# Kernel tuning notes

Hardware: AMD Instinct MI355X
Metric: run time of the kernel (lower is better)

The kernel has to match this reference:

```python
import jax, jax.numpy as jnp
import numpy as np

G, R = 2, 2          # heterogeneous graphs, meta-paths per node type
ND = NT = 3072       # drug / target node counts
NHEADS = 8
E = 100000           # DTI pairs
NEG = -1e9


def setup_inputs() -> dict:
    key = jax.random.key(0)
    ks = jax.random.split(key, 32)

    def rn(k, shape):
        return (jax.random.normal(k, shape) / np.sqrt(shape[0])).astype(jnp.float32)

    inp = {
        'x_drug': jax.random.normal(ks[0], (ND, 1024), dtype=jnp.float32),
        'x_target': jax.random.normal(ks[1], (NT, 1280), dtype=jnp.float32),
        'bias_drug': jnp.where(jax.random.uniform(ks[2], (G, R, ND, ND)) < 0.02, 0.0, NEG).astype(jnp.float32),
        'bias_target': jnp.where(jax.random.uniform(ks[3], (G, R, NT, NT)) < 0.02, 0.0, NEG).astype(jnp.float32),
        'edge_index': jax.random.randint(ks[4], (2, E), 0, ND, dtype=jnp.int64),
        'dnn_w1': rn(ks[5], (1024, 512)), 'dnn_b1': jnp.zeros((512,), jnp.float32),
        'dnn_w2': rn(ks[6], (512, 256)), 'dnn_b2': jnp.zeros((256,), jnp.float32),
        'dnn_w3': rn(ks[7], (256, 128)), 'dnn_b3': jnp.zeros((128,), jnp.float32),
        'tnn_w1': rn(ks[8], (1280, 512)), 'tnn_b1': jnp.zeros((512,), jnp.float32),
        'tnn_w2': rn(ks[9], (512, 256)), 'tnn_b2': jnp.zeros((256,), jnp.float32),
        'tnn_w3': rn(ks[10], (256, 128)), 'tnn_b3': jnp.zeros((128,), jnp.float32),
        'gat_w': rn(ks[11], (128, 16)),
        'gat_a1': rn(ks[12], (16, 1)),
        'gat_a2': rn(ks[13], (16, 1)),
        'att_w': rn(ks[14], (128, 128)), 'att_b': jnp.zeros((128,), jnp.float32),
        'att_u': rn(ks[15], (128,)),
        'a_omega': rn(ks[16], (128, 1)),
        'dec_w1': rn(ks[17], (256, 64)), 'dec_b1': jnp.zeros((64,), jnp.float32),
        'dec_w2': rn(ks[18], (64, 1)), 'dec_b2': jnp.zeros((1,), jnp.float32),
    }
    return inp


def reference(x_drug, x_target, bias_drug, bias_target, edge_index,
              dnn_w1, dnn_b1, dnn_w2, dnn_b2, dnn_w3, dnn_b3,
              tnn_w1, tnn_b1, tnn_w2, tnn_b2, tnn_w3, tnn_b3,
              gat_w, gat_a1, gat_a2, att_w, att_b, att_u, a_omega,
              dec_w1, dec_b1, dec_w2, dec_b2):

    def mlp3(x, w1, b1, w2, b2, w3, b3):  # feature NN (eval mode)
        h = jax.nn.relu(x @ w1 + b1)
        h = jax.nn.relu(h @ w2 + b2)
        return jax.nn.relu(h @ w3 + b3)

    def branch(feats, bias):
        # feats [N,128], bias [G,R,N,N]. Shared GAT layer + dropout off -> all heads identical.
        wh = feats @ gat_w                                                  # [N,16]
        e = jax.nn.leaky_relu(wh @ gat_a1 + (wh @ gat_a2).T, 0.2)           # [N,N]
        att = jax.nn.softmax(e[None, None] + bias, axis=-1)                 # [G,R,N,N]
        head = jax.nn.elu(jnp.einsum('grnm,md->grnd', att, wh))             # [G,R,N,16]
        multi = jnp.swapaxes(jnp.tile(head, (1, 1, 1, NHEADS)), 1, 2)       # [G,N,R,128]
        # semantic (meta-path) attention per graph
        v = jnp.tanh(multi @ att_w + att_b)                                 # [G,N,R,128]
        alphas = jax.nn.softmax(v @ att_u, axis=-1)                         # [G,N,R]
        per_graph = jnp.einsum('gnrh,gnr->gnh', multi, alphas)              # [G,N,128]
        # combine across heterogeneous graphs with a_omega + softmax(dim=0)
        w = jax.nn.softmax(jnp.mean(per_graph @ a_omega, axis=(1, 2)), axis=0)  # [G]
        return jnp.einsum('g,gnh->nh', w, per_graph)                        # [N,128]

    final_drug = branch(mlp3(x_drug, dnn_w1, dnn_b1, dnn_w2, dnn_b2, dnn_w3, dnn_b3), bias_drug)
    final_target = branch(mlp3(x_target, tnn_w1, tnn_b1, tnn_w2, tnn_b2, tnn_w3, tnn_b3), bias_target)

    # DTI decoder on edge pairs
    h = jnp.concatenate([final_drug[edge_index[0]], final_target[edge_index[1]]], axis=-1)  # [E,256]
    h = jax.nn.relu(h @ dec_w1 + dec_b1)
    return jax.nn.sigmoid(h @ dec_w2 + dec_b2).reshape(-1)
```

## Files before the change

### kernel.cpp

```cpp
#include <hip/hip_runtime.h>
#include <math.h>

#define ND 3072
#define EDG 100000
#define MAXE 128
#define BSL (64*8 + 16)

typedef __attribute__((ext_vector_type(8))) short short8;
typedef __attribute__((ext_vector_type(4))) float f32x4;

enum : size_t {
  OFF_FEATD = 0,
  OFF_FEATT = OFF_FEATD + 393216,
  OFF_WHD   = OFF_FEATT + 393216,
  OFF_WHT   = OFF_WHD + 49152,
  OFF_S1D   = OFF_WHT + 49152,
  OFF_S2D   = OFF_S1D + 3072,
  OFF_S1T   = OFF_S2D + 3072,
  OFF_S2T   = OFF_S1T + 3072,
  OFF_HEADD = OFF_S2T + 3072,
  OFF_HEADT = OFF_HEADD + 196608,
  OFF_PGD   = OFF_HEADT + 196608,
  OFF_PGT   = OFF_PGD + 98304,
  OFF_F16D  = OFF_PGT + 98304,
  OFF_F16T  = OFF_F16D + 49152,
  OFF_AWS   = OFF_F16T + 49152,
  OFF_W1D   = OFF_AWS + 2048,
  OFF_W1T   = OFF_W1D + 1024,
  OFF_AOM   = OFF_W1T + 1024,
  OFF_DOTSD = OFF_AOM + 16,
  OFF_DOTST = OFF_DOTSD + 6144,
  OFF_GSUM  = OFF_DOTST + 6144,
  OFF_S2MD  = OFF_GSUM + 4,
  OFF_S2MT  = OFF_S2MD + 1,
  OFF_W1DH  = ((OFF_S2MT + 4) & ~(size_t)3),
  OFF_W1DL  = OFF_W1DH + 262144,
  OFF_W1TH  = OFF_W1DL + 262144,
  OFF_W1TL  = OFF_W1TH + 327680,
  OFF_W2DH  = OFF_W1TL + 327680,
  OFF_W2DL  = OFF_W2DH + 65536,
  OFF_W2TH  = OFF_W2DL + 65536,
  OFF_W2TL  = OFF_W2TH + 65536,
  OFF_W3DH  = OFF_W2TL + 65536,
  OFF_W3DL  = OFF_W3DH + 16384,
  OFF_W3TH  = OFF_W3DL + 16384,
  OFF_W3TL  = OFF_W3TH + 16384,
  OFF_XDH   = OFF_W3TL + 16384,
  OFF_XDL   = OFF_XDH + 1572864,
  OFF_XTH   = OFF_XDL + 1572864,
  OFF_XTL   = OFF_XTH + 1966080,
  OFF_H1DH  = OFF_XTL + 1966080,
  OFF_H1DL  = OFF_H1DH + 786432,
  OFF_H1TH  = OFF_H1DL + 786432,
  OFF_H1TL  = OFF_H1TH + 786432,
  OFF_H2DH  = OFF_H1TL + 786432,
  OFF_H2DL  = OFF_H2DH + 393216,
  OFF_H2TH  = OFF_H2DL + 393216,
  OFF_H2TL  = OFF_H2TH + 393216,
  WS_GRAND  = OFF_H2TL + 393216
};

__device__ __forceinline__ ushort f2bf(float f) {
  union { float f; unsigned u; } v; v.f = f;
  unsigned r = (v.u + 0x7fffu + ((v.u >> 16) & 1u)) >> 16;
  return (ushort)r;
}
__device__ __forceinline__ float bf2f(ushort h) {
  union { float f; unsigned u; } v; v.u = ((unsigned)h) << 16;
  return v.f;
}

__global__ __launch_bounds__(256) void prep_all(
    const float* __restrict__ w1d, const float* __restrict__ w1t,
    const float* __restrict__ w2d, const float* __restrict__ w2t,
    const float* __restrict__ w3d, const float* __restrict__ w3t,
    const float* __restrict__ xd,  const float* __restrict__ xt,
    const float* __restrict__ att_w, const float* __restrict__ dec_w1,
    const float* __restrict__ a_omega, float* __restrict__ ws)
{
  const int b = blockIdx.x, t = threadIdx.x;
  if (b < 736) {
    const float* W; ushort* hi; ushort* lo; int nsh, base;
    if (b < 256)      { W=w1d; hi=(ushort*)(ws+OFF_W1DH); lo=(ushort*)(ws+OFF_W1DL); nsh=9; base=0; }
    else if (b < 576) { W=w1t; hi=(ushort*)(ws+OFF_W1TH); lo=(ushort*)(ws+OFF_W1TL); nsh=9; base=256; }
    else if (b < 640) { W=w2d; hi=(ushort*)(ws+OFF_W2DH); lo=(ushort*)(ws+OFF_W2DL); nsh=8; base=576; }
    else if (b < 704) { W=w2t; hi=(ushort*)(ws+OFF_W2TH); lo=(ushort*)(ws+OFF_W2TL); nsh=8; base=640; }
    else if (b < 720) { W=w3d; hi=(ushort*)(ws+OFF_W3DH); lo=(ushort*)(ws+OFF_W3DL); nsh=7; base=704; }
    else              { W=w3t; hi=(ushort*)(ws+OFF_W3TH); lo=(ushort*)(ws+OFF_W3TL); nsh=7; base=720; }
    const int u = (b - base)*256 + t;
    const int k8 = u >> nsh;
    const int n  = u & ((1 << nsh) - 1);
    __align__(16) ushort h8[8], l8[8];
    #pragma unroll
    for (int j2 = 0; j2 < 8; ++j2) {
      float x = W[(size_t)(k8*8 + j2) * (1 << nsh) + n];
      ushort h = f2bf(x);
      h8[j2] = h; l8[j2] = f2bf(x - bf2f(h));
    }
    *(uint4*)&hi[(size_t)u*8] = *(const uint4*)h8;
    *(uint4*)&lo[(size_t)u*8] = *(const uint4*)l8;
  } else if (b < 7648) {
    const float* X; ushort* hi; ushort* lo; int base;
    if (b < 3808) { X=xd; hi=(ushort*)(ws+OFF_XDH); lo=(ushort*)(ws+OFF_XDL); base=736; }
    else          { X=xt; hi=(ushort*)(ws+OFF_XTH); lo=(ushort*)(ws+OFF_XTL); base=3808; }
    const size_t u = ((size_t)(b-base)*256 + t)*4;
    float4 v = *(const float4*)&X[u];
    ushort4 h, l;
    h.x=f2bf(v.x); l.x=f2bf(v.x-bf2f(h.x));
    h.y=f2bf(v.y); l.y=f2bf(v.y-bf2f(h.y));
    h.z=f2bf(v.z); l.z=f2bf(v.z-bf2f(h.z));
    h.w=f2bf(v.w); l.w=f2bf(v.w-bf2f(h.w));
    *(ushort4*)&hi[u] = h; *(ushort4*)&lo[u] = l;
  } else if (b == 7648) {
    float* aws = ws + OFF_AWS; float* aom = ws + OFF_AOM;
    for (int i = t; i < 2048; i += 256) {
      int d = i >> 7, o = i & 127;
      float sum = 0.f;
      #pragma unroll
      for (int tt = 0; tt < 8; ++tt) sum += att_w[(tt*16 + d)*128 + o];
      aws[i] = sum;
    }
    if (t < 16) {
      float sum = 0.f;
      #pragma unroll
      for (int tt = 0; tt < 8; ++tt) sum += a_omega[tt*16 + t];
      aom[t] = sum;
    }
  } else {
    float* W1d = ws + OFF_W1D; float* W1t = ws + OFF_W1T;
    for (int i = t; i < 1024; i += 256) {
      int d = i >> 6, o = i & 63;
      float sd = 0.f, st = 0.f;
      #pragma unroll
      for (int tt = 0; tt < 8; ++tt) {
        sd += dec_w1[(tt*16 + d)*64 + o];
        st += dec_w1[(128 + tt*16 + d)*64 + o];
      }
      W1d[i] = sd; W1t[i] = st;
    }
  }
}

template<int BM, int EPI>
__global__ __launch_bounds__(256) void mfma_gemm2(
    const ushort* __restrict__ A0h, const ushort* __restrict__ A0l,
    const ushort* __restrict__ B0h, const ushort* __restrict__ B0l,
    const float* __restrict__ b0, float* __restrict__ C0f,
    ushort* __restrict__ C0h, ushort* __restrict__ C0l,
    const ushort* __restrict__ A1h, const ushort* __restrict__ A1l,
    const ushort* __restrict__ B1h, const ushort* __restrict__ B1l,
    const float* __restrict__ b1, float* __restrict__ C1f,
    ushort* __restrict__ C1h, ushort* __restrict__ C1l,
    int N, int K0, int K1)
{
  constexpr int ASLT = BM*8 + 16;
  constexpr int NP   = 3072 / BM;
  constexpr int AI   = BM / 32;
  __shared__ __align__(16) ushort Ah[8*ASLT], Al[8*ASLT];
  __shared__ __align__(16) ushort Bh[8*BSL], Bl[8*BSL];
  const int t = threadIdx.x;
  const int lane = t & 63, w = t >> 6;
  const int wr = w >> 1, wc = w & 1;
  const int l15 = lane & 15, l4 = lane >> 4;

  const int id = blockIdx.y * gridDim.x + blockIdx.x;
  const int xcd = id & 7;
  const int j = id >> 3;
  const int bx = j % gridDim.x;
  const int by = (j / gridDim.x) * 8 + xcd;
  const int half = by >= NP;
  const int row0 = (half ? by - NP : by) * BM;
  const int col0 = bx << 6;
  const ushort* Ahi = half ? A1h : A0h; const ushort* Alo = half ? A1l : A0l;
  const ushort* Bhi = half ? B1h : B0h; const ushort* Blo = half ? B1l : B0l;
  const float* bias = half ? b1 : b0;
  float* Cf = half ? C1f : C0f;
  ushort* Chi = half ? C1h : C0h; ushort* Clo = half ? C1l : C0l;
  const int K = half ? K1 : K0;

  f32x4 acc[AI][2] = {};

  const int arow = t >> 3;
  const int akc  = t & 7;
  const int bkc  = t >> 6;
  const int bcol = t & 63;

  uint4 sa0, sa1, sa2, sa3, sl0, sl1, sl2, sl3, sb0, sb1, sc0, sc1;

#define GLOAD(k0_) { \
    size_t g0 = (size_t)(row0 + arow) * K + (k0_) + (akc << 3); \
    sa0 = *(const uint4*)(Ahi + g0);                     sl0 = *(const uint4*)(Alo + g0); \
    sa1 = *(const uint4*)(Ahi + g0 + 32*(size_t)K);      sl1 = *(const uint4*)(Alo + g0 + 32*(size_t)K); \
    if (AI > 2) { \
      sa2 = *(const uint4*)(Ahi + g0 + 64*(size_t)K);    sl2 = *(const uint4*)(Alo + g0 + 64*(size_t)K); \
      sa3 = *(const uint4*)(Ahi + g0 + 96*(size_t)K);    sl3 = *(const uint4*)(Alo + g0 + 96*(size_t)K); \
    } \
    size_t gb0 = ((size_t)(((k0_) >> 3) + bkc    ) * N + col0 + bcol) << 3; \
    size_t gb1 = ((size_t)(((k0_) >> 3) + bkc + 4) * N + col0 + bcol) << 3; \
    sb0 = *(const uint4*)(Bhi + gb0); sc0 = *(const uint4*)(Blo + gb0); \
    sb1 = *(const uint4*)(Bhi + gb1); sc1 = *(const uint4*)(Blo + gb1); \
  }

#define LDSW() { \
    int ao = akc * ASLT + arow * 8; \
    *(uint4*)&Ah[ao      ] = sa0;  *(uint4*)&Al[ao      ] = sl0; \
    *(uint4*)&Ah[ao + 256] = sa1;  *(uint4*)&Al[ao + 256] = sl1; \
    if (AI > 2) { \
      *(uint4*)&Ah[ao + 512] = sa2;  *(uint4*)&Al[ao + 512] = sl2; \
      *(uint4*)&Ah[ao + 768] = sa3;  *(uint4*)&Al[ao + 768] = sl3; \
    } \
    int bo = bkc * BSL + bcol * 8; \
    *(uint4*)&Bh[bo        ] = sb0; *(uint4*)&Bl[bo        ] = sc0; \
    *(uint4*)&Bh[bo + 4*BSL] = sb1; *(uint4*)&Bl[bo + 4*BSL] = sc1; \
  }

  GLOAD(0);
  for (int k0 = 0; k0 < K; k0 += 64) {
    __syncthreads();
    LDSW();
    __syncthreads();
    if (k0 + 64 < K) GLOAD(k0 + 64);
    #pragma unroll
    for (int ks = 0; ks < 2; ++ks) {
      const int kch = (ks << 2) + l4;
      const int bbase = kch * BSL + ((wc << 5) + l15) * 8;
      short8 fb0 = *(const short8*)&Bh[bbase];
      short8 fb1 = *(const short8*)&Bh[bbase + 128];
      short8 gl0 = *(const short8*)&Bl[bbase];
      short8 gl1 = *(const short8*)&Bl[bbase + 128];
      #pragma unroll
      for (int m = 0; m < AI; ++m) {
        const int abase = kch * ASLT + (wr*(BM/2) + (m << 4) + l15) * 8;
        short8 fa = *(const short8*)&Ah[abase];
        short8 fl = *(const short8*)&Al[abase];
        acc[m][0] = __builtin_amdgcn_mfma_f32_16x16x32_bf16(fa, fb0, acc[m][0], 0, 0, 0);
        acc[m][0] = __builtin_amdgcn_mfma_f32_16x16x32_bf16(fa, gl0, acc[m][0], 0, 0, 0);
        acc[m][0] = __builtin_amdgcn_mfma_f32_16x16x32_bf16(fl, fb0, acc[m][0], 0, 0, 0);
        acc[m][1] = __builtin_amdgcn_mfma_f32_16x16x32_bf16(fa, fb1, acc[m][1], 0, 0, 0);
        acc[m][1] = __builtin_amdgcn_mfma_f32_16x16x32_bf16(fa, gl1, acc[m][1], 0, 0, 0);
        acc[m][1] = __builtin_amdgcn_mfma_f32_16x16x32_bf16(fl, fb1, acc[m][1], 0, 0, 0);
      }
    }
  }
#undef GLOAD
#undef LDSW

  #pragma unroll
  for (int n = 0; n < 2; ++n) {
    int col = col0 + (wc << 5) + (n << 4) + l15;
    float bb = bias[col];
    #pragma unroll
    for (int m = 0; m < AI; ++m) {
      int rowb = row0 + wr*(BM/2) + (m << 4) + (l4 << 2);
      #pragma unroll
      for (int r = 0; r < 4; ++r) {
        float v = fmaxf(acc[m][n][r] + bb, 0.f);
        size_t d = (size_t)(rowb + r) * N + col;
        if (EPI == 0) {
          Cf[d] = v;
        } else {
          ushort h = f2bf(v);
          Chi[d] = h;
          Clo[d] = f2bf(v - bf2f(h));
        }
      }
    }
  }
}

__global__ __launch_bounds__(256) void wh_kernel(const float* __restrict__ featD,
    const float* __restrict__ featT,
    const float* __restrict__ gw, const float* __restrict__ ga1, const float* __restrict__ ga2,
    float* __restrict__ ws)
{
  __shared__ float W[128*16];
  __shared__ float A1[16], A2[16];
  const int t = threadIdx.x;
  const int half = blockIdx.x >= 192;
  const float* feat = half ? featT : featD;
  float* wh = ws + (half ? OFF_WHT : OFF_WHD);
  float* s1 = ws + (half ? OFF_S1T : OFF_S1D);
  float* s2 = ws + (half ? OFF_S2T : OFF_S2D);
  const int bid = half ? blockIdx.x - 192 : blockIdx.x;
  for (int i = t; i < 2048; i += 256) W[i] = gw[i];
  if (t < 16) { A1[t] = ga1[t]; A2[t] = ga2[t]; }
  __syncthreads();
  const int n = (bid << 4) + (t >> 4);
  const int d = t & 15;
  const float* f = feat + (size_t)n * 128;
  float acc = 0.f;
  #pragma unroll 8
  for (int k = 0; k < 128; ++k) acc += f[k] * W[k*16 + d];
  wh[(size_t)n*16 + d] = acc;
  float v1 = acc * A1[d], v2 = acc * A2[d];
  #pragma unroll
  for (int off = 8; off; off >>= 1) { v1 += __shfl_xor(v1, off); v2 += __shfl_xor(v2, off); }
  if (d == 0) { s1[n] = v1; s2[n] = v2; }
}

__global__ __launch_bounds__(256) void max_kernel(float* __restrict__ ws)
{
  const int t = threadIdx.x;
  const float* s2 = ws + (blockIdx.x ? OFF_S2T : OFF_S2D);
  float* out = ws + (blockIdx.x ? OFF_S2MT : OFF_S2MD);
  float m = -INFINITY;
  for (int i = t; i < ND; i += 256) m = fmaxf(m, s2[i]);
  #pragma unroll
  for (int off = 32; off; off >>= 1) m = fmaxf(m, __shfl_xor(m, off));
  __shared__ float red[4];
  if ((t & 63) == 0) red[t >> 6] = m;
  __syncthreads();
  if (t == 0) out[0] = fmaxf(fmaxf(red[0], red[1]), fmaxf(red[2], red[3]));
}

__global__ __launch_bounds__(256) void scan_kernel(const float* __restrict__ bias_d,
    const float* __restrict__ bias_t, float* __restrict__ ws)
{
  const int half = blockIdx.x >= 3072;
  const float* bias = half ? bias_t : bias_d;
  unsigned short* idx = (unsigned short*)(ws + (half ? OFF_H1TH : OFF_H1DH));
  int* cnts = (int*)(ws + (half ? OFF_H2TH : OFF_H2DH));
  const int bid = half ? blockIdx.x - 3072 : blockIdx.x;
  const int lane = threadIdx.x & 63;
  const int row = (bid << 2) + (threadIdx.x >> 6);
  const f32x4* brow = (const f32x4*)(bias + (size_t)row * ND);
  unsigned short* ei = idx + (size_t)row * MAXE;
  const unsigned long long ltmask = (1ull << lane) - 1ull;
  int cnt = 0;
  #pragma unroll 3
  for (int i = 0; i < ND/256; ++i) {
    const int j4 = lane + (i << 6);
    f32x4 b = __builtin_nontemporal_load(&brow[j4]);
    #pragma unroll
    for (int c = 0; c < 4; ++c) {
      float bv = b[c];
      bool e = bv > -1e8f;
      unsigned long long mask = __ballot(e);
      if (e) {
        int pos = cnt + __popcll(mask & ltmask);
        if (pos < MAXE) ei[pos] = (unsigned short)((j4 << 2) + c);
      }
      cnt += __popcll(mask);
    }
  }
  if (lane == 0) cnts[row] = cnt < MAXE ? cnt : MAXE;
}

__global__ __launch_bounds__(256) void acc_kernel(float* __restrict__ ws)
{
  const int half = blockIdx.x >= 3072;
  const unsigned short* idx = (const unsigned short*)(ws + (half ? OFF_H1TH : OFF_H1DH));
  const int* cnts = (const int*)(ws + (half ? OFF_H2TH : OFF_H2DH));
  const float* s1 = ws + (half ? OFF_S1T : OFF_S1D);
  const float* s2 = ws + (half ? OFF_S2T : OFF_S2D);
  const float* s2max = ws + (half ? OFF_S2MT : OFF_S2MD);
  const float* wh = ws + (half ? OFF_WHT : OFF_WHD);
  float* head = ws + (half ? OFF_HEADT : OFF_HEADD);
  const int bid = half ? blockIdx.x - 3072 : blockIdx.x;
  const int lane = threadIdx.x & 63;
  const int row = (bid << 2) + (threadIdx.x >> 6);
  const int n = row % ND;
  const int eg = lane >> 4, d = lane & 15;
  const float s1v = s1[n];
  float mn = s1v + s2max[0];
  mn = (mn >= 0.f) ? mn : 0.2f * mn;
  const unsigned short* ei = idx + (size_t)row * MAXE;
  const int cnt = cnts[row];
  float acc = 0.f, ss = 0.f;
  if (cnt > 0) {
    for (int slot = eg; slot < cnt; slot += 4) {
      int j = ei[slot];
      float x = s1v + s2[j];
      x = (x >= 0.f) ? x : 0.2f * x;
      float p = __expf(x - mn);
      ss += p;
      acc += p * wh[j*16 + d];
    }
  } else {
    for (int j = eg; j < ND; j += 4) {
      float x = s1v + s2[j];
      x = (x >= 0.f) ? x : 0.2f * x;
      float p = __expf(x - mn);
      ss += p;
      acc += p * wh[j*16 + d];
    }
  }
  acc += __shfl_xor(acc, 16); acc += __shfl_xor(acc, 32);
  ss  += __shfl_xor(ss, 16);  ss  += __shfl_xor(ss, 32);
  if (lane < 16) {
    float v = acc / ss;
    head[(size_t)row * 16 + lane] = (v > 0.f) ? v : expm1f(v);
  }
}

__global__ __launch_bounds__(256) void sem_kernel(const float* __restrict__ att_b,
    const float* __restrict__ att_u, float* __restrict__ ws)
{
  __shared__ float AWS[2048];
  __shared__ float AB[128], AU[128], AOM[16];
  __shared__ float hsh[2][2][16];
  __shared__ float wred[4][2];
  const int half = blockIdx.x >= 3072;
  const float* head = ws + (half ? OFF_HEADT : OFF_HEADD);
  float* pg = ws + (half ? OFF_PGT : OFF_PGD);
  float* dots = ws + (half ? OFF_DOTST : OFF_DOTSD);
  const float* aws = ws + OFF_AWS;
  const float* aom = ws + OFF_AOM;
  const int bid = half ? blockIdx.x - 3072 : blockIdx.x;
  const int t = threadIdx.x;
  for (int i = t; i < 2048; i += 256) AWS[i] = aws[i];
  if (t < 128) { AB[t] = att_b[t]; AU[t] = att_u[t]; }
  if (t < 16) AOM[t] = aom[t];
  const int grp = t >> 7, o = t & 127;
  const int gn = (bid << 1) + grp;
  const int g = gn / ND, n = gn % ND;
  if (o < 32) {
    int r = o >> 4, d = o & 15;
    hsh[grp][r][d] = head[((size_t)(g*2 + r) * ND + n) * 16 + d];
  }
  __syncthreads();
  #pragma unroll
  for (int r = 0; r < 2; ++r) {
    float a = AB[o];
    #pragma unroll
    for (int d = 0; d < 16; ++d) a += hsh[grp][r][d] * AWS[d*128 + o];
    float v = tanhf(a) * AU[o];
    #pragma unroll
    for (int off = 32; off; off >>= 1) v += __shfl_xor(v, off);
    if ((t & 63) == 0) wred[t >> 6][r] = v;
  }
  __syncthreads();
  float t0 = wred[grp*2][0] + wred[grp*2 + 1][0];
  float t1 = wred[grp*2][1] + wred[grp*2 + 1][1];
  float mx = fmaxf(t0, t1);
  float e0 = __expf(t0 - mx), e1 = __expf(t1 - mx);
  float inv = 1.f / (e0 + e1);
  float a0 = e0 * inv, a1 = e1 * inv;
  if (o < 16) {
    float pv = a0 * hsh[grp][0][o] + a1 * hsh[grp][1][o];
    pg[((size_t)g * ND + n) * 16 + o] = pv;
    float contrib = pv * AOM[o];
    #pragma unroll
    for (int off = 8; off; off >>= 1) contrib += __shfl_xor(contrib, off);
    if (o == 0) dots[(size_t)g * ND + n] = contrib;
  }
}

__global__ __launch_bounds__(256) void reduce_gsum(float* __restrict__ ws)
{
  const int b = blockIdx.x, t = threadIdx.x;
  const float* dots = ws + (b < 2 ? OFF_DOTSD : OFF_DOTST) + (size_t)(b & 1) * ND;
  float v = 0.f;
  for (int i = t; i < ND; i += 256) v += dots[i];
  __shared__ float red[4];
  #pragma unroll
  for (int off = 32; off; off >>= 1) v += __shfl_xor(v, off);
  if ((t & 63) == 0) red[t >> 6] = v;
  __syncthreads();
  if (t == 0) ws[OFF_GSUM + b] = red[0] + red[1] + red[2] + red[3];
}

__global__ __launch_bounds__(256) void finalize_kernel(float* __restrict__ ws)
{
  const int half = blockIdx.x >= 192;
  const float* pg = ws + (half ? OFF_PGT : OFF_PGD);
  const float* gsum = ws + OFF_GSUM + half*2;
  float* f16 = ws + (half ? OFF_F16T : OFF_F16D);
  const int bid = half ? blockIdx.x - 192 : blockIdx.x;
  float g0 = gsum[0] * (1.f/ND), g1 = gsum[1] * (1.f/ND);
  float mx = fmaxf(g0, g1);
  float e0 = __expf(g0 - mx), e1 = __expf(g1 - mx);
  float w0 = e0 / (e0 + e1), w1 = e1 / (e0 + e1);
  int i = bid * 256 + threadIdx.x;
  if (i < ND*16) f16[i] = w0 * pg[i] + w1 * pg[ND*16 + i];
}

__global__ __launch_bounds__(256) void dec_kernel(const int* __restrict__ ei,
    const float* __restrict__ ws, const float* __restrict__ b1,
    const float* __restrict__ w2, const float* __restrict__ b2,
    float* __restrict__ out)
{
  __shared__ float WdT[64][16], WtT[64][16];
  __shared__ float B1[64], W2s[64];
  const float* f16d = ws + OFF_F16D;
  const float* f16t = ws + OFF_F16T;
  const float* W1d = ws + OFF_W1D;
  const float* W1t = ws + OFF_W1T;
  const int t = threadIdx.x;
  for (int i = t; i < 1024; i += 256) {
    int d = i >> 6, o = i & 63;
    WdT[o][d] = W1d[i];
    WtT[o][d] = W1t[i];
  }
  if (t < 64) { B1[t] = b1[t]; W2s[t] = w2[t]; }
  __syncthreads();
  const int e = blockIdx.x * 256 + t;
  if (e >= EDG) return;
  const int i0 = ei[e], i1 = ei[EDG + e];
  const float4* pd = (const float4*)(f16d + (size_t)i0 * 16);
  const float4* pt = (const float4*)(f16t + (size_t)i1 * 16);
  float4 d0 = pd[0], d1 = pd[1], d2 = pd[2], d3 = pd[3];
  float4 e0 = pt[0], e1 = pt[1], e2 = pt[2], e3 = pt[3];
  float outv = b2[0];
  #pragma unroll 4
  for (int o = 0; o < 64; ++o) {
    const float4* wd = (const float4*)&WdT[o][0];
    const float4* wt = (const float4*)&WtT[o][0];
    float4 wd0 = wd[0], wd1 = wd[1], wd2 = wd[2], wd3 = wd[3];
    float4 wt0 = wt[0], wt1 = wt[1], wt2 = wt[2], wt3 = wt[3];
    float a = B1[o];
    a += d0.x*wd0.x + d0.y*wd0.y + d0.z*wd0.z + d0.w*wd0.w;
    a += d1.x*wd1.x + d1.y*wd1.y + d1.z*wd1.z + d1.w*wd1.w;
    a += d2.x*wd2.x + d2.y*wd2.y + d2.z*wd2.z + d2.w*wd2.w;
    a += d3.x*wd3.x + d3.y*wd3.y + d3.z*wd3.z + d3.w*wd3.w;
    a += e0.x*wt0.x + e0.y*wt0.y + e0.z*wt0.z + e0.w*wt0.w;
    a += e1.x*wt1.x + e1.y*wt1.y + e1.z*wt1.z + e1.w*wt1.w;
    a += e2.x*wt2.x + e2.y*wt2.y + e2.z*wt2.z + e2.w*wt2.w;
    a += e3.x*wt3.x + e3.y*wt3.y + e3.z*wt3.z + e3.w*wt3.w;
    a = fmaxf(a, 0.f);
    outv += a * W2s[o];
  }
  out[e] = 1.f / (1.f + __expf(-outv));
}

extern "C" void kernel_launch(void* const* d_in, const int* in_sizes, int n_in,
                              void* d_out, int out_size, void* d_ws, size_t ws_size,
                              hipStream_t stream)
{
  const float* x_drug   = (const float*)d_in[0];
  const float* x_target = (const float*)d_in[1];
  const float* bias_d   = (const float*)d_in[2];
  const float* bias_t   = (const float*)d_in[3];
  const int*   ei       = (const int*)d_in[4];
  const float* dnn_w1 = (const float*)d_in[5];  const float* dnn_b1 = (const float*)d_in[6];
  const float* dnn_w2 = (const float*)d_in[7];  const float* dnn_b2 = (const float*)d_in[8];
  const float* dnn_w3 = (const float*)d_in[9];  const float* dnn_b3 = (const float*)d_in[10];
  const float* tnn_w1 = (const float*)d_in[11]; const float* tnn_b1 = (const float*)d_in[12];
  const float* tnn_w2 = (const float*)d_in[13]; const float* tnn_b2 = (const float*)d_in[14];
  const float* tnn_w3 = (const float*)d_in[15]; const float* tnn_b3 = (const float*)d_in[16];
  const float* gat_w  = (const float*)d_in[17];
  const float* gat_a1 = (const float*)d_in[18];
  const float* gat_a2 = (const float*)d_in[19];
  const float* att_w  = (const float*)d_in[20];
  const float* att_b  = (const float*)d_in[21];
  const float* att_u  = (const float*)d_in[22];
  const float* a_omega= (const float*)d_in[23];
  const float* dec_w1 = (const float*)d_in[24]; const float* dec_b1 = (const float*)d_in[25];
  const float* dec_w2 = (const float*)d_in[26]; const float* dec_b2 = (const float*)d_in[27];
  float* out = (float*)d_out;
  float* ws = (float*)d_ws;

  ushort* w1dh = (ushort*)(ws + OFF_W1DH); ushort* w1dl = (ushort*)(ws + OFF_W1DL);
  ushort* w1th = (ushort*)(ws + OFF_W1TH); ushort* w1tl = (ushort*)(ws + OFF_W1TL);
  ushort* w2dh = (ushort*)(ws + OFF_W2DH); ushort* w2dl = (ushort*)(ws + OFF_W2DL);
  ushort* w2th = (ushort*)(ws + OFF_W2TH); ushort* w2tl = (ushort*)(ws + OFF_W2TL);
  ushort* w3dh = (ushort*)(ws + OFF_W3DH); ushort* w3dl = (ushort*)(ws + OFF_W3DL);
  ushort* w3th = (ushort*)(ws + OFF_W3TH); ushort* w3tl = (ushort*)(ws + OFF_W3TL);
  ushort* xdh  = (ushort*)(ws + OFF_XDH);  ushort* xdl  = (ushort*)(ws + OFF_XDL);
  ushort* xth  = (ushort*)(ws + OFF_XTH);  ushort* xtl  = (ushort*)(ws + OFF_XTL);
  ushort* h1dh = (ushort*)(ws + OFF_H1DH); ushort* h1dl = (ushort*)(ws + OFF_H1DL);
  ushort* h1th = (ushort*)(ws + OFF_H1TH); ushort* h1tl = (ushort*)(ws + OFF_H1TL);
  ushort* h2dh = (ushort*)(ws + OFF_H2DH); ushort* h2dl = (ushort*)(ws + OFF_H2DL);
  ushort* h2th = (ushort*)(ws + OFF_H2TH); ushort* h2tl = (ushort*)(ws + OFF_H2TL);
  float* featD = ws + OFF_FEATD;
  float* featT = ws + OFF_FEATT;

  prep_all<<<7650, 256, 0, stream>>>(dnn_w1, tnn_w1, dnn_w2, tnn_w2, dnn_w3, tnn_w3,
      x_drug, x_target, att_w, dec_w1, a_omega, ws);

  mfma_gemm2<128,1><<<dim3(8,48), 256, 0, stream>>>(
      xdh, xdl, w1dh, w1dl, dnn_b1, nullptr, h1dh, h1dl,
      xth, xtl, w1th, w1tl, tnn_b1, nullptr, h1th, h1tl, 512, 1024, 1280);
  mfma_gemm2<64,1><<<dim3(4,96), 256, 0, stream>>>(
      h1dh, h1dl, w2dh, w2dl, dnn_b2, nullptr, h2dh, h2dl,
      h1th, h1tl, w2th, w2tl, tnn_b2, nullptr, h2th, h2tl, 256, 512, 512);
  mfma_gemm2<64,0><<<dim3(2,96), 256, 0, stream>>>(
      h2dh, h2dl, w3dh, w3dl, dnn_b3, featD, nullptr, nullptr,
      h2th, h2tl, w3th, w3tl, tnn_b3, featT, nullptr, nullptr, 128, 256, 256);

  wh_kernel<<<384, 256, 0, stream>>>(featD, featT, gat_w, gat_a1, gat_a2, ws);
  max_kernel<<<2, 256, 0, stream>>>(ws);

  scan_kernel<<<6144, 256, 0, stream>>>(bias_d, bias_t, ws);
  acc_kernel<<<6144, 256, 0, stream>>>(ws);

  sem_kernel<<<6144, 256, 0, stream>>>(att_b, att_u, ws);
  reduce_gsum<<<4, 256, 0, stream>>>(ws);
  finalize_kernel<<<384, 256, 0, stream>>>(ws);

  dec_kernel<<<(EDG + 255) / 256, 256, 0, stream>>>(ei, ws, dec_b1, dec_w2, dec_b2, out);
}
```

Baseline: 212.5 us.

## Use direct global-to-LDS loads in GEMM and fold tiny reduction kernels away

The split-bf16 GEMM now stages A and B tiles with global_load_lds 16-byte direct copies into LDS, using an XOR-swizzled A layout instead of register staging. Because the old double-buffered register prefetch is gone, a barrier now ends each k-step. The s2 max is computed with an order-preserving uint atomicMax inside wh_kernel, which replaces max_kernel. The gsum reduction is recomputed redundantly in every finalize block, which replaces reduce_gsum. Together these drop two launches and register-staging overhead, at the cost of losing load/compute overlap in the GEMM loop.

Result: slower. 221.6 us (+4.3%).

```diff
diff --git a/kernel.cpp b/kernel.cpp
--- a/kernel.cpp
+++ b/kernel.cpp
@@ -4,7 +4,6 @@
 #define ND 3072
 #define EDG 100000
 #define MAXE 128
-#define BSL (64*8 + 16)
 
 typedef __attribute__((ext_vector_type(8))) short short8;
 typedef __attribute__((ext_vector_type(4))) float f32x4;
@@ -30,8 +29,7 @@
   OFF_AOM   = OFF_W1T + 1024,
   OFF_DOTSD = OFF_AOM + 16,
   OFF_DOTST = OFF_DOTSD + 6144,
-  OFF_GSUM  = OFF_DOTST + 6144,
-  OFF_S2MD  = OFF_GSUM + 4,
+  OFF_S2MD  = OFF_DOTST + 6144,
   OFF_S2MT  = OFF_S2MD + 1,
   OFF_W1DH  = ((OFF_S2MT + 4) & ~(size_t)3),
   OFF_W1DL  = OFF_W1DH + 262144,
@@ -70,6 +68,12 @@
   return v.f;
 }
 
+__device__ __forceinline__ void gld16(const ushort* g, ushort* s) {
+  __builtin_amdgcn_global_load_lds(
+      (const __attribute__((address_space(1))) unsigned int*)(const void*)g,
+      (__attribute__((address_space(3))) unsigned int*)(void*)s, 16, 0, 0);
+}
+
 __global__ __launch_bounds__(256) void prep_all(
     const float* __restrict__ w1d, const float* __restrict__ w1t,
     const float* __restrict__ w2d, const float* __restrict__ w2t,
@@ -126,6 +130,10 @@
       for (int tt = 0; tt < 8; ++tt) sum += a_omega[tt*16 + t];
       aom[t] = sum;
     }
+    if (t == 0) {
+      ((unsigned*)(ws + OFF_S2MD))[0] = 0u;
+      ((unsigned*)(ws + OFF_S2MT))[0] = 0u;
+    }
   } else {
     float* W1d = ws + OFF_W1D; float* W1t = ws + OFF_W1T;
     for (int i = t; i < 1024; i += 256) {
@@ -153,11 +161,12 @@
     ushort* __restrict__ C1h, ushort* __restrict__ C1l,
     int N, int K0, int K1)
 {
-  constexpr int ASLT = BM*8 + 16;
   constexpr int NP   = 3072 / BM;
   constexpr int AI   = BM / 32;
-  __shared__ __align__(16) ushort Ah[8*ASLT], Al[8*ASLT];
-  __shared__ __align__(16) ushort Bh[8*BSL], Bl[8*BSL];
+  constexpr int AGW  = BM / 32;
+  constexpr int BSLU = 512 + 16;
+  __shared__ __align__(16) ushort Ah[BM*64], Al[BM*64];
+  __shared__ __align__(16) ushort Bh[8*BSLU], Bl[8*BSLU];
   const int t = threadIdx.x;
   const int lane = t & 63, w = t >> 6;
   const int wr = w >> 1, wc = w & 1;
@@ -180,59 +189,40 @@
 
   f32x4 acc[AI][2] = {};
 
-  const int arow = t >> 3;
-  const int akc  = t & 7;
-  const int bkc  = t >> 6;
-  const int bcol = t & 63;
-
-  uint4 sa0, sa1, sa2, sa3, sl0, sl1, sl2, sl3, sb0, sb1, sc0, sc1;
-
-#define GLOAD(k0_) { \
-    size_t g0 = (size_t)(row0 + arow) * K + (k0_) + (akc << 3); \
-    sa0 = *(const uint4*)(Ahi + g0);                     sl0 = *(const uint4*)(Alo + g0); \
-    sa1 = *(const uint4*)(Ahi + g0 + 32*(size_t)K);      sl1 = *(const uint4*)(Alo + g0 + 32*(size_t)K); \
-    if (AI > 2) { \
-      sa2 = *(const uint4*)(Ahi + g0 + 64*(size_t)K);    sl2 = *(const uint4*)(Alo + g0 + 64*(size_t)K); \
-      sa3 = *(const uint4*)(Ahi + g0 + 96*(size_t)K);    sl3 = *(const uint4*)(Alo + g0 + 96*(size_t)K); \
-    } \
-    size_t gb0 = ((size_t)(((k0_) >> 3) + bkc    ) * N + col0 + bcol) << 3; \
-    size_t gb1 = ((size_t)(((k0_) >> 3) + bkc + 4) * N + col0 + bcol) << 3; \
-    sb0 = *(const uint4*)(Bhi + gb0); sc0 = *(const uint4*)(Blo + gb0); \
-    sb1 = *(const uint4*)(Bhi + gb1); sc1 = *(const uint4*)(Blo + gb1); \
-  }
-
-#define LDSW() { \
-    int ao = akc * ASLT + arow * 8; \
-    *(uint4*)&Ah[ao      ] = sa0;  *(uint4*)&Al[ao      ] = sl0; \
-    *(uint4*)&Ah[ao + 256] = sa1;  *(uint4*)&Al[ao + 256] = sl1; \
-    if (AI > 2) { \
-      *(uint4*)&Ah[ao + 512] = sa2;  *(uint4*)&Al[ao + 512] = sl2; \
-      *(uint4*)&Ah[ao + 768] = sa3;  *(uint4*)&Al[ao + 768] = sl3; \
-    } \
-    int bo = bkc * BSL + bcol * 8; \
-    *(uint4*)&Bh[bo        ] = sb0; *(uint4*)&Bl[bo        ] = sc0; \
-    *(uint4*)&Bh[bo + 4*BSL] = sb1; *(uint4*)&Bl[bo + 4*BSL] = sc1; \
-  }
-
-  GLOAD(0);
+  const int arg = lane >> 3;
+  const int slt = lane & 7;
+  const int kcd = slt ^ arg;
+
   for (int k0 = 0; k0 < K; k0 += 64) {
+    #pragma unroll
+    for (int i = 0; i < AGW; ++i) {
+      const int g = w + (i << 2);
+      const size_t ga = (size_t)(row0 + (g << 3) + arg) * K + k0 + (kcd << 3);
+      gld16(Ahi + ga, &Ah[g << 9]);
+      gld16(Alo + ga, &Al[g << 9]);
+    }
+    #pragma unroll
+    for (int i = 0; i < 2; ++i) {
+      const int kc = w + (i << 2);
+      const size_t gb = ((size_t)((k0 >> 3) + kc) * N + col0 + lane) << 3;
+      gld16(Bhi + gb, &Bh[kc * BSLU]);
+      gld16(Blo + gb, &Bl[kc * BSLU]);
+    }
     __syncthreads();
-    LDSW();
-    __syncthreads();
-    if (k0 + 64 < K) GLOAD(k0 + 64);
     #pragma unroll
     for (int ks = 0; ks < 2; ++ks) {
       const int kch = (ks << 2) + l4;
-      const int bbase = kch * BSL + ((wc << 5) + l15) * 8;
-      short8 fb0 = *(const short8*)&Bh[bbase];
-      short8 fb1 = *(const short8*)&Bh[bbase + 128];
-      short8 gl0 = *(const short8*)&Bl[bbase];
-      short8 gl1 = *(const short8*)&Bl[bbase + 128];
+      const int bb = kch * BSLU + ((wc << 5) + l15) * 8;
+      short8 fb0 = *(const short8*)&Bh[bb];
+      short8 fb1 = *(const short8*)&Bh[bb + 128];
+      short8 gl0 = *(const short8*)&Bl[bb];
+      short8 gl1 = *(const short8*)&Bl[bb + 128];
       #pragma unroll
       for (int m = 0; m < AI; ++m) {
-        const int abase = kch * ASLT + (wr*(BM/2) + (m << 4) + l15) * 8;
-        short8 fa = *(const short8*)&Ah[abase];
-        short8 fl = *(const short8*)&Al[abase];
+        const int R = wr*(BM/2) + (m << 4) + l15;
+        const int ab = (R << 6) + ((kch ^ (R & 7)) << 3);
+        short8 fa = *(const short8*)&Ah[ab];
+        short8 fl = *(const short8*)&Al[ab];
         acc[m][0] = __builtin_amdgcn_mfma_f32_16x16x32_bf16(fa, fb0, acc[m][0], 0, 0, 0);
         acc[m][0] = __builtin_amdgcn_mfma_f32_16x16x32_bf16(fa, gl0, acc[m][0], 0, 0, 0);
         acc[m][0] = __builtin_amdgcn_mfma_f32_16x16x32_bf16(fl, fb0, acc[m][0], 0, 0, 0);
@@ -241,9 +231,8 @@
         acc[m][1] = __builtin_amdgcn_mfma_f32_16x16x32_bf16(fl, fb1, acc[m][1], 0, 0, 0);
       }
     }
-  }
-#undef GLOAD
-#undef LDSW
+    __syncthreads();
+  }
 
   #pragma unroll
   for (int n = 0; n < 2; ++n) {
@@ -281,6 +270,7 @@
   float* wh = ws + (half ? OFF_WHT : OFF_WHD);
   float* s1 = ws + (half ? OFF_S1T : OFF_S1D);
   float* s2 = ws + (half ? OFF_S2T : OFF_S2D);
+  unsigned* s2m = (unsigned*)(ws + (half ? OFF_S2MT : OFF_S2MD));
   const int bid = half ? blockIdx.x - 192 : blockIdx.x;
   for (int i = t; i < 2048; i += 256) W[i] = gw[i];
   if (t < 16) { A1[t] = ga1[t]; A2[t] = ga2[t]; }
@@ -295,22 +285,12 @@
   float v1 = acc * A1[d], v2 = acc * A2[d];
   #pragma unroll
   for (int off = 8; off; off >>= 1) { v1 += __shfl_xor(v1, off); v2 += __shfl_xor(v2, off); }
-  if (d == 0) { s1[n] = v1; s2[n] = v2; }
-}
-
-__global__ __launch_bounds__(256) void max_kernel(float* __restrict__ ws)
-{
-  const int t = threadIdx.x;
-  const float* s2 = ws + (blockIdx.x ? OFF_S2T : OFF_S2D);
-  float* out = ws + (blockIdx.x ? OFF_S2MT : OFF_S2MD);
-  float m = -INFINITY;
-  for (int i = t; i < ND; i += 256) m = fmaxf(m, s2[i]);
-  #pragma unroll
-  for (int off = 32; off; off >>= 1) m = fmaxf(m, __shfl_xor(m, off));
-  __shared__ float red[4];
-  if ((t & 63) == 0) red[t >> 6] = m;
-  __syncthreads();
-  if (t == 0) out[0] = fmaxf(fmaxf(red[0], red[1]), fmaxf(red[2], red[3]));
+  if (d == 0) {
+    s1[n] = v1; s2[n] = v2;
+    unsigned u = __float_as_uint(v2);
+    unsigned key = (u & 0x80000000u) ? ~u : (u | 0x80000000u);
+    atomicMax(s2m, key);
+  }
 }
 
 __global__ __launch_bounds__(256) void scan_kernel(const float* __restrict__ bias_d,
@@ -353,7 +333,7 @@
   const int* cnts = (const int*)(ws + (half ? OFF_H2TH : OFF_H2DH));
   const float* s1 = ws + (half ? OFF_S1T : OFF_S1D);
   const float* s2 = ws + (half ? OFF_S2T : OFF_S2D);
-  const float* s2max = ws + (half ? OFF_S2MT : OFF_S2MD);
+  const unsigned* s2mp = (const unsigned*)(ws + (half ? OFF_S2MT : OFF_S2MD));
   const float* wh = ws + (half ? OFF_WHT : OFF_WHD);
   float* head = ws + (half ? OFF_HEADT : OFF_HEADD);
   const int bid = half ? blockIdx.x - 3072 : blockIdx.x;
@@ -362,7 +342,10 @@
   const int n = row % ND;
   const int eg = lane >> 4, d = lane & 15;
   const float s1v = s1[n];
-  float mn = s1v + s2max[0];
+  const unsigned k2 = *s2mp;
+  const float s2mv = (k2 & 0x80000000u) ? __uint_as_float(k2 ^ 0x80000000u)
+                                        : __uint_as_float(~k2);
+  float mn = s1v + s2mv;
   mn = (mn >= 0.f) ? mn : 0.2f * mn;
   const unsigned short* ei = idx + (size_t)row * MAXE;
   const int cnt = cnts[row];
@@ -446,32 +429,27 @@
   }
 }
 
-__global__ __launch_bounds__(256) void reduce_gsum(float* __restrict__ ws)
-{
-  const int b = blockIdx.x, t = threadIdx.x;
-  const float* dots = ws + (b < 2 ? OFF_DOTSD : OFF_DOTST) + (size_t)(b & 1) * ND;
-  float v = 0.f;
-  for (int i = t; i < ND; i += 256) v += dots[i];
-  __shared__ float red[4];
-  #pragma unroll
-  for (int off = 32; off; off >>= 1) v += __shfl_xor(v, off);
-  if ((t & 63) == 0) red[t >> 6] = v;
-  __syncthreads();
-  if (t == 0) ws[OFF_GSUM + b] = red[0] + red[1] + red[2] + red[3];
-}
-
 __global__ __launch_bounds__(256) void finalize_kernel(float* __restrict__ ws)
 {
   const int half = blockIdx.x >= 192;
   const float* pg = ws + (half ? OFF_PGT : OFF_PGD);
-  const float* gsum = ws + OFF_GSUM + half*2;
+  const float* dots = ws + (half ? OFF_DOTST : OFF_DOTSD);
   float* f16 = ws + (half ? OFF_F16T : OFF_F16D);
   const int bid = half ? blockIdx.x - 192 : blockIdx.x;
-  float g0 = gsum[0] * (1.f/ND), g1 = gsum[1] * (1.f/ND);
+  const int t = threadIdx.x;
+  float v0 = 0.f, v1 = 0.f;
+  for (int i = t; i < ND; i += 256) { v0 += dots[i]; v1 += dots[ND + i]; }
+  #pragma unroll
+  for (int off = 32; off; off >>= 1) { v0 += __shfl_xor(v0, off); v1 += __shfl_xor(v1, off); }
+  __shared__ float red[4][2];
+  if ((t & 63) == 0) { red[t >> 6][0] = v0; red[t >> 6][1] = v1; }
+  __syncthreads();
+  float g0 = (red[0][0] + red[1][0] + red[2][0] + red[3][0]) * (1.f/ND);
+  float g1 = (red[0][1] + red[1][1] + red[2][1] + red[3][1]) * (1.f/ND);
   float mx = fmaxf(g0, g1);
   float e0 = __expf(g0 - mx), e1 = __expf(g1 - mx);
   float w0 = e0 / (e0 + e1), w1 = e1 / (e0 + e1);
-  int i = bid * 256 + threadIdx.x;
+  int i = bid * 256 + t;
   if (i < ND*16) f16[i] = w0 * pg[i] + w1 * pg[ND*16 + i];
 }
 
@@ -579,13 +557,11 @@
       h2th, h2tl, w3th, w3tl, tnn_b3, featT, nullptr, nullptr, 128, 256, 256);
 
   wh_kernel<<<384, 256, 0, stream>>>(featD, featT, gat_w, gat_a1, gat_a2, ws);
-  max_kernel<<<2, 256, 0, stream>>>(ws);
 
   scan_kernel<<<6144, 256, 0, stream>>>(bias_d, bias_t, ws);
   acc_kernel<<<6144, 256, 0, stream>>>(ws);
 
   sem_kernel<<<6144, 256, 0, stream>>>(att_b, att_u, ws);
-  reduce_gsum<<<4, 256, 0, stream>>>(ws);
   finalize_kernel<<<384, 256, 0, stream>>>(ws);
 
   dec_kernel<<<(EDG + 255) / 256, 256, 0, stream>>>(ei, ws, dec_b1, dec_w2, dec_b2, out);
```
